# Optimization experiments

Measured on AMD Instinct MI355X. Metric: run time of the kernel, lower is better.

Reference implementation:

```python
import jax, jax.numpy as jnp
import numpy as np
import math

N_HEAD = 16
ROPE_BASE = 10000.0


def _rope(x):
    # x: [B, S, H, Dh]
    S, d = x.shape[1], x.shape[-1]
    inv_freq = 1.0 / (ROPE_BASE ** (jnp.arange(0, d, 2, dtype=jnp.float32) / d))
    t = jnp.arange(S, dtype=jnp.float32)
    freqs = jnp.einsum('i,j->ij', t, inv_freq)              # [S, d/2]
    emb = jnp.concatenate([freqs, freqs], axis=-1)          # [S, d]
    cos = jnp.cos(emb)[None, :, None, :]
    sin = jnp.sin(emb)[None, :, None, :]
    x1, x2 = jnp.split(x, 2, axis=-1)
    x_rot = jnp.concatenate([-x2, x1], axis=-1)
    return x * cos + x_rot * sin


def setup_inputs() -> dict:
    key = jax.random.key(0)
    ks = jax.random.split(key, 6)
    B, S, D = 2, 2048, 1024
    x = jax.random.normal(ks[0], (B, S, D), dtype=jnp.float32)
    w = lambda k: jax.random.normal(k, (D, D), dtype=jnp.float32) * 0.02
    return {'x': x, 'wq': w(ks[1]), 'wk': w(ks[2]), 'wv': w(ks[3]),
            'wg': w(ks[4]), 'wo': w(ks[5])}


def reference(x, wq, wk, wv, wg, wo):
    B, S, D = x.shape
    H = N_HEAD
    Dh = D // H

    # projections (torch Linear: y = x @ W^T)
    q = (x @ wq.T).reshape(B, S, H, Dh)
    k = (x @ wk.T).reshape(B, S, H, Dh)
    v = (x @ wv.T).reshape(B, S, H, Dh)

    q = _rope(q)
    k = _rope(k)

    q = q.transpose(0, 2, 1, 3)  # [B,H,S,Dh]
    k = k.transpose(0, 2, 1, 3)
    v = v.transpose(0, 2, 1, 3)

    # per-head exponential decay mask (causal)
    idx = jnp.arange(S)
    d_mask = jnp.tril(idx[:, None] - idx[None, :]).astype(jnp.float32)  # [S,S]
    gamma = 1.0 - jnp.exp2(-5.0 - jnp.arange(H, dtype=jnp.float32))     # [H]
    causal = jnp.tril(jnp.ones((S, S), dtype=jnp.float32))
    decay_matrix = jnp.power(gamma[:, None, None], d_mask) * causal     # [H,S,S]

    retention = jnp.einsum('bhsd,bhtd->bhst', q, k) / math.sqrt(Dh)
    retention = retention * decay_matrix[None]                          # [B,H,S,S]

    out = jnp.einsum('bhst,bhtd->bhsd', retention, v)
    out = out.transpose(0, 2, 1, 3).reshape(B, S, D)

    g = jax.nn.silu(x @ wg.T)
    return (out * g) @ wo.T
```

## Files before the change

kernel.cpp:

```cpp
#include <hip/hip_runtime.h>
#include <hip/hip_bf16.h>

typedef unsigned short u16;
typedef unsigned int u32;
typedef __attribute__((ext_vector_type(8))) short short8;
typedef __attribute__((ext_vector_type(4))) float f32x4;

#define S_LEN 2048
#define D_DIM 1024
#define NH    16
#define DH    64
#define B_SZ  2
#define M_ROWS (B_SZ * S_LEN)
#define NCHUNK (S_LEN / 64)

__device__ __forceinline__ u16 f2bf(float f) {
  u32 u = __float_as_uint(f);
  u += 0x7FFFu + ((u >> 16) & 1u);
  return (u16)(u >> 16);
}
__device__ __forceinline__ float bf2f(u16 u) {
  return __uint_as_float(((u32)u) << 16);
}
__device__ __forceinline__ u32 pack_bf2(float lo, float hi) {
  __hip_bfloat162 p = __float22bfloat162_rn(make_float2(lo, hi));
  u32 r;
  __builtin_memcpy(&r, &p, 4);
  return r;
}

__device__ __forceinline__ void gll16(const void* g, void* l) {
  __builtin_amdgcn_global_load_lds((const __attribute__((address_space(1))) u32*)g,
                                   (__attribute__((address_space(3))) u32*)l,
                                   16, 0, 0);
}

#define SP1() __builtin_amdgcn_s_setprio(1)
#define SP0() __builtin_amdgcn_s_setprio(0)
#define BAR() __builtin_amdgcn_s_barrier()
#define LGKM0() do { asm volatile("s_waitcnt lgkmcnt(0)" ::: "memory"); \
                     __builtin_amdgcn_sched_barrier(0); } while (0)

__global__ __launch_bounds__(256) void prep_kernel(
    const float* __restrict__ x,
    const float* __restrict__ wq, const float* __restrict__ wk,
    const float* __restrict__ wv, const float* __restrict__ wg,
    const float* __restrict__ wo,
    u16* __restrict__ xb, u16* __restrict__ wcat, float2* __restrict__ rope)
{
  const int bid = blockIdx.x, tid = threadIdx.x;
  if (bid < 4096) {
    const int i = bid * 256 + tid;
    const float4 v = ((const float4*)x)[i];
    u32* d = (u32*)xb;
    d[2 * i]     = (u32)f2bf(v.x) | ((u32)f2bf(v.y) << 16);
    d[2 * i + 1] = (u32)f2bf(v.z) | ((u32)f2bf(v.w) << 16);
  } else if (bid < 9216) {
    const int t = bid - 4096;
    const int seg = t >> 10;
    const float* src = seg == 0 ? wq : seg == 1 ? wk : seg == 2 ? wv : seg == 3 ? wg : wo;
    const int i = (t & 1023) * 256 + tid;
    const float4 v = ((const float4*)src)[i];
    u32* d = (u32*)(wcat + (size_t)seg * D_DIM * D_DIM);
    d[2 * i]     = (u32)f2bf(v.x) | ((u32)f2bf(v.y) << 16);
    d[2 * i + 1] = (u32)f2bf(v.z) | ((u32)f2bf(v.w) << 16);
  } else {
    const int i = (bid - 9216) * 256 + tid;
    const int s = i >> 5, j = i & 31;
    float inv = exp2f(-(float)j * (13.287712379549449f / 32.f));
    float fr = (float)s * inv;
    rope[i] = make_float2(cosf(fr), sinf(fr));
  }
}

__global__ __launch_bounds__(512, 2) void proj_kernel(
    const u16* __restrict__ xb, const u16* __restrict__ wcat,
    u16* __restrict__ qb, u16* __restrict__ kb, u16* __restrict__ kT,
    u16* __restrict__ vT, u16* __restrict__ gb,
    const float2* __restrict__ rope)
{
  __shared__ u16 lds[65536];
  const int tid = threadIdx.x, lane = tid & 63, wid = tid >> 6;
  const int wm = wid >> 2, wn = wid & 3;
  const int l15 = lane & 15, l4 = lane >> 4;

  const int bid = blockIdx.x;
  const int sw = (bid & 7) * 32 + (bid >> 3);
  const int m0 = (sw & 15) * 256;
  const int n0 = (sw >> 4) * 256;

  f32x4 acc[8][4];
  #pragma unroll
  for (int m = 0; m < 8; ++m)
    #pragma unroll
    for (int n = 0; n < 4; ++n)
      acc[m][n] = (f32x4){0.f, 0.f, 0.f, 0.f};

  short8 a[4][2], b0[2][2], b1[2][2];

  auto stA = [&](int t, int h) {
    u16* dst = lds + ((t & 1) * 2 + h) * 8192;
    const u16* src = xb + (size_t)(m0 + h * 128) * D_DIM + t * 64;
    #pragma unroll
    for (int j = 0; j < 2; ++j) {
      const int c = tid + j * 512, row = c >> 3, ch = c & 7;
      gll16(src + (size_t)row * D_DIM + ((ch ^ (row & 7)) << 3), dst + c * 8);
    }
  };
  auto stB = [&](int t, int h) {
    u16* dst = lds + 32768 + ((t & 1) * 2 + h) * 8192;
    const u16* src = wcat + (size_t)(n0 + h * 128) * D_DIM + t * 64;
    #pragma unroll
    for (int j = 0; j < 2; ++j) {
      const int c = tid + j * 512, row = c >> 3, ch = c & 7;
      gll16(src + (size_t)row * D_DIM + ((ch ^ (row & 7)) << 3), dst + c * 8);
    }
  };
  auto ldA = [&](int d, int mh) {
    const u16* base = lds + (d * 2 + wm) * 8192;
    #pragma unroll
    for (int m = 0; m < 4; ++m) {
      const int lr = mh * 64 + m * 16 + l15;
      #pragma unroll
      for (int kk = 0; kk < 2; ++kk)
        a[m][kk] = *(const short8*)(base + lr * 64 + (((kk * 4 + l4) ^ (lr & 7)) << 3));
    }
  };
  auto ldB = [&](short8 (&b)[2][2], int d, int nh) {
    const u16* base = lds + 32768 + (d * 2 + (wn >> 1)) * 8192;
    #pragma unroll
    for (int j = 0; j < 2; ++j) {
      const int lr = (wn & 1) * 64 + (nh * 2 + j) * 16 + l15;
      #pragma unroll
      for (int kk = 0; kk < 2; ++kk)
        b[j][kk] = *(const short8*)(base + lr * 64 + (((kk * 4 + l4) ^ (lr & 7)) << 3));
    }
  };
  auto quad = [&](int mh, int nh, short8 (&b)[2][2]) {
    #pragma unroll
    for (int m = 0; m < 4; ++m)
      #pragma unroll
      for (int j = 0; j < 2; ++j)
        #pragma unroll
        for (int kk = 0; kk < 2; ++kk)
          acc[mh * 4 + m][nh * 2 + j] =
              __builtin_amdgcn_mfma_f32_16x16x32_bf16(a[m][kk], b[j][kk],
                                                      acc[mh * 4 + m][nh * 2 + j], 0, 0, 0);
  };

  stB(0, 0); stA(0, 0); stB(0, 1); stA(0, 1); stB(1, 0); stB(1, 1);
  asm volatile("s_waitcnt vmcnt(4)" ::: "memory");
  BAR();

  for (int i = 0; i < 8; ++i) {
    const int t1 = 2 * i + 1, t2 = 2 * i + 2, t3 = 2 * i + 3;
    ldA(0, 0); ldB(b0, 0, 0); ldB(b1, 0, 1);
    stA(t1, 0); stA(t1, 1);
    asm volatile("s_waitcnt lgkmcnt(8)" ::: "memory");
    BAR(); LGKM0();
    SP1(); quad(0, 0, b0); quad(0, 1, b1); SP0();
    BAR();
    ldA(0, 1);
    if (t2 < 16) { stB(t2, 0); stA(t2, 0); }
    asm volatile("s_waitcnt lgkmcnt(4)" ::: "memory");
    BAR(); LGKM0();
    SP1(); quad(1, 0, b0); quad(1, 1, b1); SP0();
    if (i == 7) asm volatile("s_waitcnt vmcnt(0)" ::: "memory");
    else        asm volatile("s_waitcnt vmcnt(4)" ::: "memory");
    BAR();
    ldA(1, 0); ldB(b0, 1, 0); ldB(b1, 1, 1);
    if (t2 < 16) { stB(t2, 1); stA(t2, 1); }
    asm volatile("s_waitcnt lgkmcnt(8)" ::: "memory");
    BAR(); LGKM0();
    SP1(); quad(0, 0, b0); quad(0, 1, b1); SP0();
    BAR();
    ldA(1, 1);
    if (t3 < 16) { stB(t3, 0); stB(t3, 1); }
    asm volatile("s_waitcnt lgkmcnt(4)" ::: "memory");
    BAR(); LGKM0();
    SP1(); quad(1, 0, b0); quad(1, 1, b1); SP0();
    if (i < 7) asm volatile("s_waitcnt vmcnt(4)" ::: "memory");
    else       asm volatile("s_waitcnt vmcnt(0)" ::: "memory");
    BAR();
  }

  const int gcol = n0 + wn * 64;
  const int z = gcol >> 10;
  const int hh = (gcol >> 6) & (NH - 1);
  const int mcol = gcol & (D_DIM - 1);
  const int rbase = m0 + wm * 128 + l4 * 4;
  const float lgh = log2f(1.f - exp2f(-5.f - (float)hh));

  if (z <= 1) {
    u16* dst = z ? kb : qb;
    const float slg  = z ? -lgh : lgh;
    const float base = z ? 1.f : 0.125f;
    #pragma unroll
    for (int m = 0; m < 8; ++m) {
      float o1v[2][4], o2v[2][4];
      #pragma unroll
      for (int r = 0; r < 4; ++r) {
        const int row = rbase + m * 16 + r;
        const int s = row & (S_LEN - 1);
        const float sc = base * exp2f((float)(s & 63) * slg);
        #pragma unroll
        for (int n = 0; n < 2; ++n) {
          const int dh0 = n * 16 + l15;
          const float2 cs = rope[s * 32 + dh0];
          const float x1 = acc[m][n][r], x2 = acc[m][n + 2][r];
          const float o1 = (x1 * cs.x - x2 * cs.y) * sc;
          const float o2 = (x2 * cs.x + x1 * cs.y) * sc;
          dst[(size_t)row * D_DIM + mcol + n * 16 + l15]       = f2bf(o1);
          dst[(size_t)row * D_DIM + mcol + (n + 2) * 16 + l15] = f2bf(o2);
          o1v[n][r] = o1; o2v[n][r] = o2;
        }
      }
      if (z == 1) {
        const int row0 = rbase + m * 16;
        const int bb = row0 >> 11, sr = row0 & (S_LEN - 1);
        #pragma unroll
        for (int n = 0; n < 2; ++n) {
          const int dh0 = n * 16 + l15;
          const uint2 p1 = make_uint2(pack_bf2(o1v[n][0], o1v[n][1]), pack_bf2(o1v[n][2], o1v[n][3]));
          const uint2 p2 = make_uint2(pack_bf2(o2v[n][0], o2v[n][1]), pack_bf2(o2v[n][2], o2v[n][3]));
          *(uint2*)(kT + (size_t)((bb * NH + hh) * DH + dh0) * S_LEN + sr)      = p1;
          *(uint2*)(kT + (size_t)((bb * NH + hh) * DH + dh0 + 32) * S_LEN + sr) = p2;
        }
      }
    }
  } else if (z == 2) {
    #pragma unroll
    for (int m = 0; m < 8; ++m) {
      const int row0 = rbase + m * 16;
      const int bb = row0 >> 11, sr = row0 & (S_LEN - 1);
      #pragma unroll
      for (int n = 0; n < 4; ++n) {
        const int dh = n * 16 + l15;
        const uint2 p = make_uint2(pack_bf2(acc[m][n][0], acc[m][n][1]),
                                   pack_bf2(acc[m][n][2], acc[m][n][3]));
        *(uint2*)(vT + (size_t)((bb * NH + hh) * DH + dh) * S_LEN + sr) = p;
      }
    }
  } else {
    #pragma unroll
    for (int m = 0; m < 8; ++m)
      #pragma unroll
      for (int n = 0; n < 4; ++n)
        #pragma unroll
        for (int r = 0; r < 4; ++r) {
          const int row = rbase + m * 16 + r;
          const float v = acc[m][n][r];
          gb[(size_t)row * D_DIM + mcol + n * 16 + l15] = f2bf(v / (1.f + __expf(-v)));
        }
  }
}

template<int BM, int BN, int WPM, int WPN>
__device__ __forceinline__ void gemm_bk32(const u16* __restrict__ A,
                                          const u16* __restrict__ W,
                                          const int m0, const int n0,
                                          u16* lds,
                                          f32x4 (&acc)[BM / (WPM * 16)][BN / (WPN * 16)])
{
  constexpr int T   = WPM * WPN * 64;
  constexpr int MR  = BM / (WPM * 16);
  constexpr int NR  = BN / (WPN * 16);
  constexpr int ALD = BM * 32;
  constexpr int BLD = BN * 32;
  constexpr int BUF = ALD + BLD;
  constexpr int NK  = D_DIM / 32;

  const int tid  = threadIdx.x;
  const int lane = tid & 63, wid = tid >> 6;
  const int wm = wid / WPN, wn = wid % WPN;
  const int l15 = lane & 15, l4 = lane >> 4;

  #pragma unroll
  for (int m = 0; m < MR; ++m)
    #pragma unroll
    for (int n = 0; n < NR; ++n)
      acc[m][n] = (f32x4){0.f, 0.f, 0.f, 0.f};

  auto stage = [&](int kt) {
    const int k0 = kt * 32;
    u16* la = lds + (kt & 3) * BUF;
    u16* lb = la + ALD;
    #pragma unroll
    for (int j = 0; j < BM * 4 / T; ++j) {
      const int c = tid + j * T;
      gll16(A + (size_t)(m0 + (c >> 2)) * D_DIM + k0 + (c & 3) * 8, la + c * 8);
    }
    #pragma unroll
    for (int j = 0; j < BN * 4 / T; ++j) {
      const int c = tid + j * T;
      gll16(W + (size_t)(n0 + (c >> 2)) * D_DIM + k0 + (c & 3) * 8, lb + c * 8);
    }
  };

  stage(0);
  stage(1);
  asm volatile("s_waitcnt vmcnt(4)" ::: "memory");
  BAR();
  __builtin_amdgcn_sched_barrier(0);

  for (int i = 0; i < NK; ++i) {
    if (i + 2 < NK) stage(i + 2);
    const u16* la = lds + (i & 3) * BUF + (wm * (BM / WPM) + l15) * 32 + l4 * 8;
    const u16* lb = lds + (i & 3) * BUF + ALD + (wn * (BN / WPN) + l15) * 32 + l4 * 8;
    short8 av[MR], bv[NR];
    #pragma unroll
    for (int m = 0; m < MR; ++m) av[m] = *(const short8*)(la + m * 16 * 32);
    #pragma unroll
    for (int n = 0; n < NR; ++n) bv[n] = *(const short8*)(lb + n * 16 * 32);
    SP1();
    #pragma unroll
    for (int m = 0; m < MR; ++m)
      #pragma unroll
      for (int n = 0; n < NR; ++n)
        acc[m][n] = __builtin_amdgcn_mfma_f32_16x16x32_bf16(av[m], bv[n], acc[m][n], 0, 0, 0);
    SP0();
    if (i + 2 < NK) asm volatile("s_waitcnt vmcnt(4)" ::: "memory");
    else            asm volatile("s_waitcnt vmcnt(0)" ::: "memory");
    BAR();
    __builtin_amdgcn_sched_barrier(0);
  }
}

__global__ __launch_bounds__(256) void chunk_accum(
    const u16* __restrict__ kT, const u16* __restrict__ vT,
    u16* __restrict__ At)
{
  const int tid = threadIdx.x, lane = tid & 63, w = tid >> 6;
  const int l15 = lane & 15, l4 = lane >> 4;
  const int bh = blockIdx.x >> 5, c = blockIdx.x & 31;

  short8 a[2], bfr[2][4];
  #pragma unroll
  for (int kk = 0; kk < 2; ++kk) {
    a[kk] = *(const short8*)(vT + (size_t)(bh * DH + w * 16 + l15) * S_LEN + c * 64 + kk * 32 + l4 * 8);
    #pragma unroll
    for (int n = 0; n < 4; ++n)
      bfr[kk][n] = *(const short8*)(kT + (size_t)(bh * DH + n * 16 + l15) * S_LEN + c * 64 + kk * 32 + l4 * 8);
  }
  f32x4 acc[4];
  #pragma unroll
  for (int n = 0; n < 4; ++n) acc[n] = (f32x4){0.f, 0.f, 0.f, 0.f};
  #pragma unroll
  for (int kk = 0; kk < 2; ++kk)
    #pragma unroll
    for (int n = 0; n < 4; ++n)
      acc[n] = __builtin_amdgcn_mfma_f32_16x16x32_bf16(a[kk], bfr[kk][n], acc[n], 0, 0, 0);

  u16* dst = At + ((size_t)(bh * NCHUNK + c)) * 4096;
  #pragma unroll
  for (int n = 0; n < 4; ++n)
    #pragma unroll
    for (int r = 0; r < 4; ++r)
      dst[(w * 16 + l4 * 4 + r) * 64 + n * 16 + l15] = f2bf(acc[n][r]);
}

__global__ __launch_bounds__(256) void chunk_scan(
    const u16* __restrict__ At, u16* __restrict__ St)
{
  const int gid = blockIdx.x * 256 + threadIdx.x;
  const int bh = gid >> 12, e = gid & 4095;
  const int h = bh & (NH - 1);
  const float lg = log2f(1.f - exp2f(-5.f - (float)h));
  const float gC = exp2f(64.f * lg);
  const u16* src = At + (size_t)bh * NCHUNK * 4096 + e;
  u16* dst = St + (size_t)bh * NCHUNK * 4096 + e;
  float s = 0.f;
  for (int c = 0; c < NCHUNK; ++c) {
    const float a = bf2f(src[(size_t)c * 4096]);
    dst[(size_t)c * 4096] = f2bf(s);
    s = gC * (s + a);
  }
}

__global__ __launch_bounds__(256) void chunk_out(
    const u16* __restrict__ qb, const u16* __restrict__ kb,
    const u16* __restrict__ vT, const u16* __restrict__ St,
    const u16* __restrict__ gb, u16* __restrict__ ob)
{
  __shared__ u16 Ps[4][16 * 64];

  const int tid = threadIdx.x, lane = tid & 63, w = tid >> 6;
  const int l15 = lane & 15, l4 = lane >> 4;
  const int bh = blockIdx.x >> 5, c = blockIdx.x & 31;
  const int b = bh >> 4, h = bh & (NH - 1);
  const int q0 = c * 64 + w * 16;

  short8 qfr[2], kf[2][4], vf[2][4], sf[2][4];
  #pragma unroll
  for (int kk = 0; kk < 2; ++kk) {
    qfr[kk] = *(const short8*)(qb + (size_t)(b * S_LEN + q0 + l15) * D_DIM + h * DH + kk * 32 + l4 * 8);
    #pragma unroll
    for (int t = 0; t < 4; ++t)
      kf[kk][t] = *(const short8*)(kb + (size_t)(b * S_LEN + c * 64 + t * 16 + l15) * D_DIM + h * DH + kk * 32 + l4 * 8);
    #pragma unroll
    for (int n = 0; n < 4; ++n) {
      vf[kk][n] = *(const short8*)(vT + (size_t)(bh * DH + n * 16 + l15) * S_LEN + c * 64 + kk * 32 + l4 * 8);
      sf[kk][n] = *(const short8*)(St + ((size_t)(bh * NCHUNK + c)) * 4096 + (n * 16 + l15) * 64 + kk * 32 + l4 * 8);
    }
  }

  f32x4 st[4];
  #pragma unroll
  for (int tf = 0; tf < 4; ++tf) st[tf] = (f32x4){0.f, 0.f, 0.f, 0.f};
  #pragma unroll
  for (int kk = 0; kk < 2; ++kk)
    #pragma unroll
    for (int tf = 0; tf < 4; ++tf)
      st[tf] = __builtin_amdgcn_mfma_f32_16x16x32_bf16(kf[kk][tf], qfr[kk], st[tf], 0, 0, 0);

  f32x4 acc[4];
  #pragma unroll
  for (int n = 0; n < 4; ++n) acc[n] = (f32x4){0.f, 0.f, 0.f, 0.f};
  #pragma unroll
  for (int kk = 0; kk < 2; ++kk)
    #pragma unroll
    for (int n = 0; n < 4; ++n)
      acc[n] = __builtin_amdgcn_mfma_f32_16x16x32_bf16(qfr[kk], sf[kk][n], acc[n], 0, 0, 0);

  u16* const psw = &Ps[w][0];
  const int qq = w * 16 + l15;
  #pragma unroll
  for (int tf = 0; tf < 4; ++tf) {
    const int tb = tf * 16 + l4 * 4;
    const float v0 = (tb + 0 <= qq) ? st[tf][0] : 0.f;
    const float v1 = (tb + 1 <= qq) ? st[tf][1] : 0.f;
    const float v2 = (tb + 2 <= qq) ? st[tf][2] : 0.f;
    const float v3 = (tb + 3 <= qq) ? st[tf][3] : 0.f;
    const uint2 u = make_uint2(pack_bf2(v0, v1), pack_bf2(v2, v3));
    const int boff = l15 * 128 + ((tf * 32 + l4 * 8) ^ ((l15 & 7) << 4));
    *(uint2*)((char*)psw + boff) = u;
  }

  #pragma unroll
  for (int kk = 0; kk < 2; ++kk) {
    const int boff = l15 * 128 + ((kk * 64 + l4 * 16) ^ ((l15 & 7) << 4));
    const short8 pa = *(const short8*)((const char*)psw + boff);
    #pragma unroll
    for (int n = 0; n < 4; ++n)
      acc[n] = __builtin_amdgcn_mfma_f32_16x16x32_bf16(pa, vf[kk][n], acc[n], 0, 0, 0);
  }

  #pragma unroll
  for (int n = 0; n < 4; ++n)
    #pragma unroll
    for (int r = 0; r < 4; ++r) {
      const size_t idx = (size_t)(b * S_LEN + q0 + l4 * 4 + r) * D_DIM + h * DH + n * 16 + l15;
      ob[idx] = f2bf(acc[n][r] * bf2f(gb[idx]));
    }
}

__global__ __launch_bounds__(256, 2) void final_kernel(
    const u16* __restrict__ ob, const u16* __restrict__ wob,
    float* __restrict__ out)
{
  __shared__ u16 lds[4 * (128 * 32 + 128 * 32)];
  f32x4 acc[4][4];
  const int bid = blockIdx.x;
  const int sw = (bid & 7) * 32 + (bid >> 3);
  const int n0 = (sw & 7) * 128;
  const int m0 = (sw >> 3) * 128;
  gemm_bk32<128, 128, 2, 2>(ob, wob, m0, n0, lds, acc);

  const int lane = threadIdx.x & 63, wid = threadIdx.x >> 6;
  const int wm = wid >> 1, wn = wid & 1;
  const int rbase = m0 + wm * 64 + (lane >> 4) * 4;
  const int cbase = n0 + wn * 64 + (lane & 15);
  #pragma unroll
  for (int m = 0; m < 4; ++m)
    #pragma unroll
    for (int n = 0; n < 4; ++n)
      #pragma unroll
      for (int r = 0; r < 4; ++r)
        out[(size_t)(rbase + m * 16 + r) * D_DIM + cbase + n * 16] = acc[m][n][r];
}

extern "C" void kernel_launch(void* const* d_in, const int* in_sizes, int n_in,
                              void* d_out, int out_size, void* d_ws, size_t ws_size,
                              hipStream_t stream) {
  (void)in_sizes; (void)n_in; (void)out_size; (void)ws_size;
  const float* x  = (const float*)d_in[0];
  const float* wq = (const float*)d_in[1];
  const float* wk = (const float*)d_in[2];
  const float* wv = (const float*)d_in[3];
  const float* wg = (const float*)d_in[4];
  const float* wo = (const float*)d_in[5];
  float* out = (float*)d_out;

  char* ws = (char*)d_ws;
  const size_t SZ_X = (size_t)M_ROWS * D_DIM * 2;
  const size_t SZ_W = (size_t)D_DIM * D_DIM * 2;
  u16* xb   = (u16*)(ws);
  u16* wcat = (u16*)(ws + SZ_X);
  u16* wob  = (u16*)(ws + SZ_X + 4 * SZ_W);
  u16* qb   = (u16*)(ws + 1 * SZ_X + 5 * SZ_W);
  u16* kb   = (u16*)(ws + 2 * SZ_X + 5 * SZ_W);
  u16* vT   = (u16*)(ws + 3 * SZ_X + 5 * SZ_W);
  u16* gb   = (u16*)(ws + 4 * SZ_X + 5 * SZ_W);
  u16* kT   = (u16*)(ws + 5 * SZ_X + 5 * SZ_W);
  u16* ob   = kT;
  float2* rope = (float2*)(ws + 6 * SZ_X + 5 * SZ_W);
  u16* St   = (u16*)(ws);
  u16* At   = (u16*)(ws + SZ_X);

  prep_kernel<<<dim3(9472), 256, 0, stream>>>(x, wq, wk, wv, wg, wo, xb, wcat, rope);

  proj_kernel<<<dim3(256), 512, 0, stream>>>(xb, wcat, qb, kb, kT, vT, gb, rope);

  chunk_accum<<<dim3(B_SZ * NH * NCHUNK), 256, 0, stream>>>(kT, vT, At);
  chunk_scan<<<dim3(B_SZ * NH * 4096 / 256), 256, 0, stream>>>(At, St);
  chunk_out<<<dim3(B_SZ * NH * NCHUNK), 256, 0, stream>>>(qb, kb, vT, St, gb, ob);

  final_kernel<<<dim3(256), 256, 0, stream>>>(ob, wob, out);
}
```

Before: 103.4 us.

## Retile projection GEMM to 256x128 blocks with triple-buffered LDS pipeline

The fused QKVG projection GEMM now uses 256x128 output tiles instead of 256x256 and launches 512 blocks instead of 256. Each of the 8 waves owns a 64x64 subtile. The hand-interleaved half-tile double-buffer schedule is replaced by a simpler fully unrolled loop with a 3-stage LDS ring, prefetching two k-steps ahead and using one barrier per step. The aim is better CU coverage and latency hiding with fewer barriers. In exchange, operand reuse per block drops and LDS use grows to 144KB, which may limit how many blocks fit per CU.

After: 111.7 us. 1.08x slower.

```diff
diff --git a/kernel.cpp b/kernel.cpp
--- a/kernel.cpp
+++ b/kernel.cpp
@@ -79,108 +79,79 @@
     u16* __restrict__ vT, u16* __restrict__ gb,
     const float2* __restrict__ rope)
 {
-  __shared__ u16 lds[65536];
+  __shared__ u16 lds[73728];
   const int tid = threadIdx.x, lane = tid & 63, wid = tid >> 6;
-  const int wm = wid >> 2, wn = wid & 3;
+  const int wm = wid >> 1, wn = wid & 1;
   const int l15 = lane & 15, l4 = lane >> 4;
 
   const int bid = blockIdx.x;
-  const int sw = (bid & 7) * 32 + (bid >> 3);
+  const int sw = (bid & 7) * 64 + (bid >> 3);
   const int m0 = (sw & 15) * 256;
-  const int n0 = (sw >> 4) * 256;
-
-  f32x4 acc[8][4];
-  #pragma unroll
-  for (int m = 0; m < 8; ++m)
+  const int n0 = (sw >> 4) * 128;
+
+  f32x4 acc[4][4];
+  #pragma unroll
+  for (int m = 0; m < 4; ++m)
     #pragma unroll
     for (int n = 0; n < 4; ++n)
       acc[m][n] = (f32x4){0.f, 0.f, 0.f, 0.f};
 
-  short8 a[4][2], b0[2][2], b1[2][2];
-
-  auto stA = [&](int t, int h) {
-    u16* dst = lds + ((t & 1) * 2 + h) * 8192;
-    const u16* src = xb + (size_t)(m0 + h * 128) * D_DIM + t * 64;
+  auto stA = [&](int t) {
+    u16* dst = lds + (t % 3) * 16384;
+    const u16* src = xb + (size_t)m0 * D_DIM + t * 64;
+    #pragma unroll
+    for (int j = 0; j < 4; ++j) {
+      const int c = tid + j * 512, row = c >> 3, ch = c & 7;
+      gll16(src + (size_t)row * D_DIM + ((ch ^ (row & 7)) << 3), dst + c * 8);
+    }
+  };
+  auto stB = [&](int t) {
+    u16* dst = lds + 49152 + (t % 3) * 8192;
+    const u16* src = wcat + (size_t)n0 * D_DIM + t * 64;
     #pragma unroll
     for (int j = 0; j < 2; ++j) {
       const int c = tid + j * 512, row = c >> 3, ch = c & 7;
       gll16(src + (size_t)row * D_DIM + ((ch ^ (row & 7)) << 3), dst + c * 8);
     }
   };
-  auto stB = [&](int t, int h) {
-    u16* dst = lds + 32768 + ((t & 1) * 2 + h) * 8192;
-    const u16* src = wcat + (size_t)(n0 + h * 128) * D_DIM + t * 64;
-    #pragma unroll
-    for (int j = 0; j < 2; ++j) {
-      const int c = tid + j * 512, row = c >> 3, ch = c & 7;
-      gll16(src + (size_t)row * D_DIM + ((ch ^ (row & 7)) << 3), dst + c * 8);
-    }
-  };
-  auto ldA = [&](int d, int mh) {
-    const u16* base = lds + (d * 2 + wm) * 8192;
-    #pragma unroll
-    for (int m = 0; m < 4; ++m) {
-      const int lr = mh * 64 + m * 16 + l15;
-      #pragma unroll
-      for (int kk = 0; kk < 2; ++kk)
-        a[m][kk] = *(const short8*)(base + lr * 64 + (((kk * 4 + l4) ^ (lr & 7)) << 3));
-    }
-  };
-  auto ldB = [&](short8 (&b)[2][2], int d, int nh) {
-    const u16* base = lds + 32768 + (d * 2 + (wn >> 1)) * 8192;
-    #pragma unroll
-    for (int j = 0; j < 2; ++j) {
-      const int lr = (wn & 1) * 64 + (nh * 2 + j) * 16 + l15;
-      #pragma unroll
-      for (int kk = 0; kk < 2; ++kk)
-        b[j][kk] = *(const short8*)(base + lr * 64 + (((kk * 4 + l4) ^ (lr & 7)) << 3));
-    }
-  };
-  auto quad = [&](int mh, int nh, short8 (&b)[2][2]) {
-    #pragma unroll
-    for (int m = 0; m < 4; ++m)
-      #pragma unroll
-      for (int j = 0; j < 2; ++j)
+
+  stA(0); stB(0); stA(1); stB(1);
+  asm volatile("s_waitcnt vmcnt(6)" ::: "memory");
+  __builtin_amdgcn_sched_barrier(0);
+  BAR();
+
+  #pragma unroll
+  for (int t = 0; t < 16; ++t) {
+    if (t + 2 < 16) { stA(t + 2); stB(t + 2); }
+    const u16* abase = lds + (t % 3) * 16384;
+    const u16* bbase = lds + 49152 + (t % 3) * 8192;
+    short8 af[2][4], bf[2][4];
+    #pragma unroll
+    for (int kk = 0; kk < 2; ++kk) {
+      #pragma unroll
+      for (int m = 0; m < 4; ++m) {
+        const int lr = wm * 64 + m * 16 + l15;
+        af[kk][m] = *(const short8*)(abase + lr * 64 + (((kk * 4 + l4) ^ (lr & 7)) << 3));
+      }
+      #pragma unroll
+      for (int n = 0; n < 4; ++n) {
+        const int lr = wn * 64 + n * 16 + l15;
+        bf[kk][n] = *(const short8*)(bbase + lr * 64 + (((kk * 4 + l4) ^ (lr & 7)) << 3));
+      }
+    }
+    LGKM0();
+    SP1();
+    #pragma unroll
+    for (int kk = 0; kk < 2; ++kk)
+      #pragma unroll
+      for (int m = 0; m < 4; ++m)
         #pragma unroll
-        for (int kk = 0; kk < 2; ++kk)
-          acc[mh * 4 + m][nh * 2 + j] =
-              __builtin_amdgcn_mfma_f32_16x16x32_bf16(a[m][kk], b[j][kk],
-                                                      acc[mh * 4 + m][nh * 2 + j], 0, 0, 0);
-  };
-
-  stB(0, 0); stA(0, 0); stB(0, 1); stA(0, 1); stB(1, 0); stB(1, 1);
-  asm volatile("s_waitcnt vmcnt(4)" ::: "memory");
-  BAR();
-
-  for (int i = 0; i < 8; ++i) {
-    const int t1 = 2 * i + 1, t2 = 2 * i + 2, t3 = 2 * i + 3;
-    ldA(0, 0); ldB(b0, 0, 0); ldB(b1, 0, 1);
-    stA(t1, 0); stA(t1, 1);
-    asm volatile("s_waitcnt lgkmcnt(8)" ::: "memory");
-    BAR(); LGKM0();
-    SP1(); quad(0, 0, b0); quad(0, 1, b1); SP0();
-    BAR();
-    ldA(0, 1);
-    if (t2 < 16) { stB(t2, 0); stA(t2, 0); }
-    asm volatile("s_waitcnt lgkmcnt(4)" ::: "memory");
-    BAR(); LGKM0();
-    SP1(); quad(1, 0, b0); quad(1, 1, b1); SP0();
-    if (i == 7) asm volatile("s_waitcnt vmcnt(0)" ::: "memory");
-    else        asm volatile("s_waitcnt vmcnt(4)" ::: "memory");
-    BAR();
-    ldA(1, 0); ldB(b0, 1, 0); ldB(b1, 1, 1);
-    if (t2 < 16) { stB(t2, 1); stA(t2, 1); }
-    asm volatile("s_waitcnt lgkmcnt(8)" ::: "memory");
-    BAR(); LGKM0();
-    SP1(); quad(0, 0, b0); quad(0, 1, b1); SP0();
-    BAR();
-    ldA(1, 1);
-    if (t3 < 16) { stB(t3, 0); stB(t3, 1); }
-    asm volatile("s_waitcnt lgkmcnt(4)" ::: "memory");
-    BAR(); LGKM0();
-    SP1(); quad(1, 0, b0); quad(1, 1, b1); SP0();
-    if (i < 7) asm volatile("s_waitcnt vmcnt(4)" ::: "memory");
-    else       asm volatile("s_waitcnt vmcnt(0)" ::: "memory");
+        for (int n = 0; n < 4; ++n)
+          acc[m][n] = __builtin_amdgcn_mfma_f32_16x16x32_bf16(af[kk][m], bf[kk][n], acc[m][n], 0, 0, 0);
+    SP0();
+    if (t <= 13)      asm volatile("s_waitcnt vmcnt(6)" ::: "memory");
+    else if (t == 14) asm volatile("s_waitcnt vmcnt(0)" ::: "memory");
+    __builtin_amdgcn_sched_barrier(0);
     BAR();
   }
 
@@ -188,7 +159,7 @@
   const int z = gcol >> 10;
   const int hh = (gcol >> 6) & (NH - 1);
   const int mcol = gcol & (D_DIM - 1);
-  const int rbase = m0 + wm * 128 + l4 * 4;
+  const int rbase = m0 + wm * 64 + l4 * 4;
   const float lgh = log2f(1.f - exp2f(-5.f - (float)hh));
 
   if (z <= 1) {
@@ -196,7 +167,7 @@
     const float slg  = z ? -lgh : lgh;
     const float base = z ? 1.f : 0.125f;
     #pragma unroll
-    for (int m = 0; m < 8; ++m) {
+    for (int m = 0; m < 4; ++m) {
       float o1v[2][4], o2v[2][4];
       #pragma unroll
       for (int r = 0; r < 4; ++r) {
@@ -230,7 +201,7 @@
     }
   } else if (z == 2) {
     #pragma unroll
-    for (int m = 0; m < 8; ++m) {
+    for (int m = 0; m < 4; ++m) {
       const int row0 = rbase + m * 16;
       const int bb = row0 >> 11, sr = row0 & (S_LEN - 1);
       #pragma unroll
@@ -243,7 +214,7 @@
     }
   } else {
     #pragma unroll
-    for (int m = 0; m < 8; ++m)
+    for (int m = 0; m < 4; ++m)
       #pragma unroll
       for (int n = 0; n < 4; ++n)
         #pragma unroll
@@ -509,7 +480,7 @@
 
   prep_kernel<<<dim3(9472), 256, 0, stream>>>(x, wq, wk, wv, wg, wo, xb, wcat, rope);
 
-  proj_kernel<<<dim3(256), 512, 0, stream>>>(xb, wcat, qb, kb, kT, vT, gb, rope);
+  proj_kernel<<<dim3(512), 512, 0, stream>>>(xb, wcat, qb, kb, kT, vT, gb, rope);
 
   chunk_accum<<<dim3(B_SZ * NH * NCHUNK), 256, 0, stream>>>(kT, vT, At);
   chunk_scan<<<dim3(B_SZ * NH * 4096 / 256), 256, 0, stream>>>(At, St);
```
